# Kernel tuning notes

Hardware: AMD Instinct MI355X
Metric: run time of the kernel (lower is better)

## Reference

```python
import jax, jax.numpy as jnp
import numpy as np

VOCAB = 32000
HID = 512
T_IN = 128
T_OUT = 128
BATCH = 32


def gru_scan(xs, h0, W, U, bi, br):
    """Keras GRUCell (reset_after=True) over time.
    xs: [T, B, H] inputs; h0: [B, H]; W: [H, 3H]; U: [H, 3H]; bi, br: [3H].
    Returns (h_final [B,H], hs [T,B,H])."""
    # input projections for all timesteps at once
    x_proj = jnp.einsum('tbh,hg->tbg', xs, W) + bi  # [T, B, 3H]

    def step(h, xp):
        rec = h @ U + br                      # [B, 3H]
        xz, xr, xh = jnp.split(xp, 3, axis=-1)
        rz, rr, rh = jnp.split(rec, 3, axis=-1)
        z = jax.nn.sigmoid(xz + rz)
        r = jax.nn.sigmoid(xr + rr)
        hh = jnp.tanh(xh + r * rh)
        h_new = z * h + (1.0 - z) * hh
        return h_new, h_new

    h_final, hs = jax.lax.scan(step, h0, x_proj)
    return h_final, hs


def setup_inputs() -> dict:
    key = jax.random.key(0)
    ks = jax.random.split(key, 12)
    s = 0.05
    return {
        'inputs': jax.random.randint(ks[0], (BATCH, T_IN), 0, VOCAB, dtype=jnp.int64 if jax.config.jax_enable_x64 else jnp.int32),
        'emb': jax.random.normal(ks[1], (VOCAB, HID), jnp.float32) * s,
        'enc_W': jax.random.normal(ks[2], (HID, 3 * HID), jnp.float32) * s,
        'enc_U': jax.random.normal(ks[3], (HID, 3 * HID), jnp.float32) * s,
        'enc_bi': jnp.zeros((3 * HID,), jnp.float32),
        'enc_br': jnp.zeros((3 * HID,), jnp.float32),
        'dec_W': jax.random.normal(ks[4], (HID, 3 * HID), jnp.float32) * s,
        'dec_U': jax.random.normal(ks[5], (HID, 3 * HID), jnp.float32) * s,
        'dec_bi': jnp.zeros((3 * HID,), jnp.float32),
        'dec_br': jnp.zeros((3 * HID,), jnp.float32),
        'w_relu': jax.random.normal(ks[6], (HID, HID), jnp.float32) * s,
        'b_relu': jnp.zeros((HID,), jnp.float32),
        'w_out': jax.random.normal(ks[7], (HID, VOCAB), jnp.float32) * s,
        'b_out': jnp.zeros((VOCAB,), jnp.float32),
    }


def reference(inputs, emb, enc_W, enc_U, enc_bi, enc_br,
              dec_W, dec_U, dec_bi, dec_br, w_relu, b_relu, w_out, b_out):
    B = inputs.shape[0]
    # Embedding lookup: [B, T_in, H] -> time-major [T_in, B, H]
    x = jnp.transpose(emb[inputs], (1, 0, 2))
    h0 = jnp.zeros((B, HID), jnp.float32)
    # Encoder GRU -> final state
    h_enc, _ = gru_scan(x, h0, enc_W, enc_U, enc_bi, enc_br)
    # RepeatVector: decoder input is encoder state at every target step
    dec_in = jnp.broadcast_to(h_enc[None], (T_OUT, B, HID))
    # Decoder GRU with fresh zero state, return sequences
    _, hs = gru_scan(dec_in, h0, dec_W, dec_U, dec_bi, dec_br)  # [T_out, B, H]
    hs = jnp.transpose(hs, (1, 0, 2))  # [B, T_out, H]
    # TimeDistributed Dense+relu, then Dense+softmax over vocab
    h1 = jax.nn.relu(jnp.einsum('bth,hk->btk', hs, w_relu) + b_relu)
    logits = jnp.einsum('bth,hv->btv', h1, w_out) + b_out
    return jax.nn.softmax(logits, axis=-1)
```

## Files before the change

### kernel.cpp

```cpp
#include <hip/hip_runtime.h>
#include <stdint.h>

#define VOCAB 32000
#define HID   512
#define G3    1536
#define TT    128
#define BB    32
#define NROW  4096
#define NCB   250

typedef __attribute__((ext_vector_type(8))) short short8;
typedef __attribute__((ext_vector_type(4))) short short4v;
typedef __attribute__((ext_vector_type(4))) float f32x4;
typedef __attribute__((ext_vector_type(2))) unsigned long long u64x2;

__device__ __forceinline__ unsigned short f2bf(float f) {
  unsigned int u = __builtin_bit_cast(unsigned int, f);
  u += 0x7fffu + ((u >> 16) & 1u);
  return (unsigned short)(u >> 16);
}
__device__ __forceinline__ float bf2f(unsigned short s) {
  unsigned int u = ((unsigned int)s) << 16;
  return __builtin_bit_cast(float, u);
}
__device__ __forceinline__ void gload16(const void* g, void* l) {
  __builtin_amdgcn_global_load_lds(
      (const __attribute__((address_space(1))) unsigned int*)g,
      (__attribute__((address_space(3))) unsigned int*)l, 16, 0, 0);
}
__device__ __forceinline__ unsigned long long AL64(const unsigned long long* p) {
  return __hip_atomic_load(p, __ATOMIC_RELAXED, __HIP_MEMORY_SCOPE_AGENT);
}
__device__ __forceinline__ unsigned int AL32(const unsigned int* p) {
  return __hip_atomic_load(p, __ATOMIC_RELAXED, __HIP_MEMORY_SCOPE_AGENT);
}
__device__ __forceinline__ void AS64(unsigned long long* p, unsigned long long v) {
  __hip_atomic_store(p, v, __ATOMIC_RELAXED, __HIP_MEMORY_SCOPE_AGENT);
}
__device__ __forceinline__ void AS32(unsigned int* p, unsigned int v) {
  __hip_atomic_store(p, v, __ATOMIC_RELAXED, __HIP_MEMORY_SCOPE_AGENT);
}

__global__ void transpose_bf16_k(const float* __restrict__ src,
                                 unsigned short* __restrict__ dst,
                                 int K, int N) {
  __shared__ float t[64][65];
  int k0 = blockIdx.x * 64, n0 = blockIdx.y * 64;
  int c = threadIdx.x & 15, rr = threadIdx.x >> 4;
#pragma unroll
  for (int i = 0; i < 4; ++i) {
    float4 v = *(const float4*)(src + (size_t)(k0 + rr + 16 * i) * N + n0 + c * 4);
    t[rr + 16 * i][c * 4 + 0] = v.x;
    t[rr + 16 * i][c * 4 + 1] = v.y;
    t[rr + 16 * i][c * 4 + 2] = v.z;
    t[rr + 16 * i][c * 4 + 3] = v.w;
  }
  __syncthreads();
#pragma unroll
  for (int i = 0; i < 4; ++i) {
    short4v o;
#pragma unroll
    for (int j = 0; j < 4; ++j) o[j] = (short)f2bf(t[c * 4 + j][rr + 16 * i]);
    *(short4v*)(dst + (size_t)(n0 + rr + 16 * i) * K + k0 + c * 4) = o;
  }
}

__global__ void embed_k(const int* __restrict__ inputs,
                        const float* __restrict__ emb,
                        unsigned short* __restrict__ xb) {
  int r = blockIdx.x;
  int t = r >> 5, b = r & 31;
  int idx = inputs[b * TT + t];
  const float* src = emb + (size_t)idx * HID;
  unsigned short* dst = xb + (size_t)r * HID;
  int j = threadIdx.x * 4;
  float4 v = *(const float4*)(src + j);
  short4v o;
  o[0] = (short)f2bf(v.x); o[1] = (short)f2bf(v.y);
  o[2] = (short)f2bf(v.z); o[3] = (short)f2bf(v.w);
  *(short4v*)(dst + j) = o;
}

template<int MODE>
__launch_bounds__(256)
__global__ void gemm_bt(const unsigned short* __restrict__ A,
                        const unsigned short* __restrict__ BT,
                        const float* __restrict__ bias,
                        void* __restrict__ Cv,
                        float* __restrict__ partials,
                        int M, int N, int K) {
  __shared__ unsigned short As[8192];
  __shared__ unsigned short Bs[8192];
  __shared__ float rsum[2][128];
  int tid = threadIdx.x;
  int l = tid & 63;
  int w = tid >> 6;
  int wm = w >> 1, wn = w & 1;

  int nwg = (int)(gridDim.x * gridDim.y);
  int id = (int)(blockIdx.y * gridDim.x + blockIdx.x);
  int nid = (id & 7) * (nwg >> 3) + (id >> 3);
  int bx = nid & 31, by = nid >> 5;
  int row0 = bx * 128;
  int col0 = by * 128;

  int sr = (w << 5) + (l >> 3);
  int sg = ((l & 7) ^ ((l >> 3) & 7)) << 3;
  const unsigned short* Ag = A  + (size_t)(row0 + sr) * K + sg;
  const unsigned short* Bg = BT + (size_t)(col0 + sr) * K + sg;

  int cA = l & 15, q = l >> 4, x7 = l & 7;
  const char* asp = (const char*)As;
  const char* bsp = (const char*)Bs;

  f32x4 acc[4][4];
#pragma unroll
  for (int m = 0; m < 4; ++m)
#pragma unroll
    for (int n = 0; n < 4; ++n) acc[m][n] = (f32x4){0.f, 0.f, 0.f, 0.f};

  for (int k0 = 0; k0 < K; k0 += 64) {
    if (k0) __syncthreads();
#pragma unroll
    for (int i = 0; i < 4; ++i) {
      gload16(Ag + (size_t)(i * 8) * K + k0, As + ((w << 2) + i) * 512);
      gload16(Bg + (size_t)(i * 8) * K + k0, Bs + ((w << 2) + i) * 512);
    }
    __syncthreads();
#pragma unroll
    for (int kk = 0; kk < 2; ++kk) {
      int sl = (((kk << 2) + q) ^ x7) << 4;
      short8 af[4], bf[4];
#pragma unroll
      for (int m = 0; m < 4; ++m)
        af[m] = *(const short8*)(asp + (wm * 64 + m * 16 + cA) * 128 + sl);
#pragma unroll
      for (int n = 0; n < 4; ++n)
        bf[n] = *(const short8*)(bsp + (wn * 64 + n * 16 + cA) * 128 + sl);
#pragma unroll
      for (int m = 0; m < 4; ++m)
#pragma unroll
        for (int n = 0; n < 4; ++n)
          acc[m][n] = __builtin_amdgcn_mfma_f32_16x16x32_bf16(af[m], bf[n],
                                                              acc[m][n], 0, 0, 0);
    }
  }

  if (MODE == 0 || MODE == 1) {
#pragma unroll
    for (int m = 0; m < 4; ++m)
#pragma unroll
      for (int n = 0; n < 4; ++n) {
        int col = col0 + wn * 64 + n * 16 + cA;
        float bv = bias[col];
#pragma unroll
        for (int r = 0; r < 4; ++r) {
          int row = row0 + wm * 64 + m * 16 + q * 4 + r;
          float v = acc[m][n][r] + bv;
          if (MODE == 0)
            ((float*)Cv)[(size_t)row * N + col] = v;
          else
            ((unsigned short*)Cv)[(size_t)row * N + col] = f2bf(fmaxf(v, 0.f));
        }
      }
  } else {
    float ps[4][4];
#pragma unroll
    for (int m = 0; m < 4; ++m)
#pragma unroll
      for (int r = 0; r < 4; ++r) ps[m][r] = 0.f;
#pragma unroll
    for (int m = 0; m < 4; ++m)
#pragma unroll
      for (int n = 0; n < 4; ++n) {
        int col = col0 + wn * 64 + n * 16 + cA;
        float bv = bias[col];
#pragma unroll
        for (int r = 0; r < 4; ++r) {
          int row = row0 + wm * 64 + m * 16 + q * 4 + r;
          float lv = acc[m][n][r] + bv;
          float v = __expf(lv);
          if (MODE == 2)
            ((float*)Cv)[(size_t)row * N + col] = v;
          else
            ((unsigned short*)Cv)[(size_t)row * N + col] = f2bf(lv);
          ps[m][r] += v;
        }
      }
#pragma unroll
    for (int mask = 1; mask < 16; mask <<= 1)
#pragma unroll
      for (int m = 0; m < 4; ++m)
#pragma unroll
        for (int r = 0; r < 4; ++r)
          ps[m][r] += __shfl_xor(ps[m][r], mask, 64);
    if (cA == 0) {
#pragma unroll
      for (int m = 0; m < 4; ++m)
#pragma unroll
        for (int r = 0; r < 4; ++r)
          rsum[wn][wm * 64 + m * 16 + q * 4 + r] = ps[m][r];
    }
    __syncthreads();
    if (tid < 128)
      partials[(size_t)by * NROW + row0 + tid] = rsum[0][tid] + rsum[1][tid];
  }
}

__launch_bounds__(256)
__global__ void gemm_small_k(const unsigned short* __restrict__ A,
                             const unsigned short* __restrict__ B,
                             const float* __restrict__ bias,
                             float* __restrict__ C,
                             int M, int N, int K) {
  __shared__ unsigned short As[64][56];
  __shared__ unsigned short Bs[64][56];
  int tid = threadIdx.x;
  int lane = tid & 63;
  int w = tid >> 6;
  int wm = w >> 1, wn = w & 1;
  int row0 = blockIdx.x * 64;
  int n0 = blockIdx.y * 64;
  f32x4 acc[2][2];
#pragma unroll
  for (int a = 0; a < 2; ++a)
#pragma unroll
    for (int c = 0; c < 2; ++c) acc[a][c] = (f32x4){0.f, 0.f, 0.f, 0.f};
  for (int k0 = 0; k0 < K; k0 += 32) {
    {
      int row = tid >> 2;
      int kg = (tid & 3) * 8;
      short8 v = {};
      if (row0 + row < M)
        v = *(const short8*)(A + (size_t)(row0 + row) * K + k0 + kg);
      *(short8*)&As[row][kg] = v;
    }
    {
      int k = tid >> 3;
      int ng = (tid & 7) * 8;
      short8 v = *(const short8*)(B + (size_t)(k0 + k) * N + n0 + ng);
#pragma unroll
      for (int qq = 0; qq < 8; ++qq) Bs[ng + qq][k] = (unsigned short)v[qq];
    }
    __syncthreads();
    int kb = (lane >> 4) * 8;
    short8 af0 = *(const short8*)&As[wm * 32 + (lane & 15)][kb];
    short8 af1 = *(const short8*)&As[wm * 32 + 16 + (lane & 15)][kb];
    short8 bf0 = *(const short8*)&Bs[wn * 32 + (lane & 15)][kb];
    short8 bf1 = *(const short8*)&Bs[wn * 32 + 16 + (lane & 15)][kb];
    acc[0][0] = __builtin_amdgcn_mfma_f32_16x16x32_bf16(af0, bf0, acc[0][0], 0, 0, 0);
    acc[0][1] = __builtin_amdgcn_mfma_f32_16x16x32_bf16(af0, bf1, acc[0][1], 0, 0, 0);
    acc[1][0] = __builtin_amdgcn_mfma_f32_16x16x32_bf16(af1, bf0, acc[1][0], 0, 0, 0);
    acc[1][1] = __builtin_amdgcn_mfma_f32_16x16x32_bf16(af1, bf1, acc[1][1], 0, 0, 0);
    __syncthreads();
  }
#pragma unroll
  for (int tm = 0; tm < 2; ++tm)
#pragma unroll
    for (int tn = 0; tn < 2; ++tn) {
      int col = n0 + wn * 32 + tn * 16 + (lane & 15);
      float bv = bias[col];
#pragma unroll
      for (int r = 0; r < 4; ++r) {
        int row = row0 + wm * 32 + tm * 16 + ((lane >> 4) * 4) + r;
        if (row < M)
          C[(size_t)row * N + col] = acc[tm][tn][r] + bv;
      }
    }
}

template<int XPT>
__device__ void gru_body(char* smem, const float* __restrict__ U,
                         const float* __restrict__ xp, const float* __restrict__ br,
                         unsigned short* __restrict__ hpub,
                         unsigned int* __restrict__ flags) {
  unsigned short* ub = (unsigned short*)smem;
  char* hbase = smem + 49152;
  float (*recbuf)[32][16] = (float (*)[32][16])(smem + 81920);
  int tid = threadIdx.x;
  int lane = tid & 63;
  int w = tid >> 6;
  int g = blockIdx.x;

  for (int idx = tid; idx < 16 * 3 * 64 * 8; idx += 512) {
    int i = idx & 7;
    int l = (idx >> 3) & 63;
    int rem = idx >> 9;
    int nt = rem % 3;
    int ks = rem / 3;
    int k = ks * 32 + ((l >> 4) * 8) + i;
    int col = nt * 512 + g * 16 + (l & 15);
    ub[idx] = f2bf(U[(size_t)k * G3 + col]);
  }
  int b = tid >> 4, j = tid & 15;
  float br_z = br[g * 16 + j];
  float br_r = br[512 + g * 16 + j];
  float br_h = br[1024 + g * 16 + j];
  float hreg = 0.f;
  __syncthreads();

  int mt = w / 3, nt = w % 3;
  for (int t = 0; t < TT; ++t) {
    size_t xbase = ((size_t)(t * XPT + b)) * G3 + g * 16 + j;
    float xz = xp[xbase], xr = xp[xbase + 512], xh = xp[xbase + 1024];

    float rz, rr, rh;
    if (t == 0) {
      rz = 0.f; rr = 0.f; rh = 0.f;
    } else {
      {
        const unsigned long long* hr =
            (const unsigned long long*)(hpub + ((t & 1) ? 16384 : 0));
        int r = tid >> 4, s = tid & 15;
        unsigned long long av[8];
#pragma unroll
        for (int k = 0; k < 4; ++k) {
          const unsigned long long* p = hr + (size_t)r * 128 + (s + 16 * k) * 2;
          av[2 * k] = AL64(p);
          av[2 * k + 1] = AL64(p + 1);
        }
        int rx = (r & 7) << 4;
#pragma unroll
        for (int k = 0; k < 4; ++k) {
          int wb = (r * 1024 + (s + 16 * k) * 16) ^ rx;
          u64x2 v;
          v[0] = av[2 * k];
          v[1] = av[2 * k + 1];
          *(u64x2*)(hbase + wb) = v;
        }
      }
      __syncthreads();

      if (w < 6) {
        int arow = mt * 16 + (lane & 15);
        int rx = (arow & 7) << 4;
        int abase = arow * 1024 + (lane >> 4) * 16;
        f32x4 acc0 = (f32x4){0.f, 0.f, 0.f, 0.f};
        f32x4 acc1 = (f32x4){0.f, 0.f, 0.f, 0.f};
#pragma unroll
        for (int ks = 0; ks < 8; ++ks) {
          short8 af0 = *(const short8*)(hbase + ((abase + ks * 64) ^ rx));
          short8 af1 = *(const short8*)(hbase + ((abase + (ks + 8) * 64) ^ rx));
          short8 bf0 = *(const short8*)&ub[((ks * 3 + nt) * 64 + lane) * 8];
          short8 bf1 = *(const short8*)&ub[(((ks + 8) * 3 + nt) * 64 + lane) * 8];
          acc0 = __builtin_amdgcn_mfma_f32_16x16x32_bf16(af0, bf0, acc0, 0, 0, 0);
          acc1 = __builtin_amdgcn_mfma_f32_16x16x32_bf16(af1, bf1, acc1, 0, 0, 0);
        }
        f32x4 acc = acc0 + acc1;
#pragma unroll
        for (int r = 0; r < 4; ++r)
          recbuf[nt][mt * 16 + (lane >> 4) * 4 + r][lane & 15] = acc[r];
      }
      __syncthreads();
      rz = recbuf[0][b][j];
      rr = recbuf[1][b][j];
      rh = recbuf[2][b][j];
    }

    float z = 1.f / (1.f + __expf(-(xz + rz + br_z)));
    float rg = 1.f / (1.f + __expf(-(xr + rr + br_r)));
    float pre = xh + rg * (rh + br_h);
    pre = fminf(fmaxf(pre, -15.f), 15.f);
    float e2 = __expf(2.f * pre);
    float hh = (e2 - 1.f) / (e2 + 1.f);
    hreg = z * hreg + (1.f - z) * hh;
    unsigned short hb = f2bf(hreg);

    unsigned int hv = (unsigned int)hb;
    unsigned int p1 = (unsigned int)__shfl_xor((int)hv, 1, 64);
    unsigned long long lo = (unsigned long long)((hv & 0xffffu) | (p1 << 16));
    unsigned long long hi =
        (unsigned long long)(unsigned int)__shfl_xor((int)(unsigned int)lo, 2, 64);
    if ((j & 3) == 0) {
      unsigned long long pk = (lo & 0xffffffffull) | (hi << 32);
      AS64((unsigned long long*)(hpub + (((t + 1) & 1) ? 16384 : 0) +
                                 b * HID + g * 16 + j), pk);
    }

    if (t + 1 < TT) {
      asm volatile("s_waitcnt vmcnt(0)" ::: "memory");
      __syncthreads();
      if (tid == 0)
        AS32(flags + g * 32, (unsigned)(t + 1));
      if (lane < 32) {
        const unsigned int* fp = flags + lane * 32;
        while (AL32(fp) < (unsigned)(t + 1)) {}
      }
    }
  }
}

__launch_bounds__(512)
__global__ void gru_k(const float* __restrict__ U,
                      const float* __restrict__ xp,
                      const float* __restrict__ br,
                      unsigned short* __restrict__ hpub,
                      unsigned short* __restrict__ hsout,
                      unsigned int* __restrict__ flags) {
  __shared__ unsigned short ub[16 * 3 * 64 * 8];
  __shared__ unsigned short hbuf[16384];
  __shared__ float recbuf[3][32][16];
  int tid = threadIdx.x;
  int lane = tid & 63;
  int w = tid >> 6;
  int g = blockIdx.x;
  char* hbase = (char*)hbuf;

  for (int idx = tid; idx < 16 * 3 * 64 * 8; idx += 512) {
    int i = idx & 7;
    int l = (idx >> 3) & 63;
    int rem = idx >> 9;
    int nt = rem % 3;
    int ks = rem / 3;
    int k = ks * 32 + ((l >> 4) * 8) + i;
    int col = nt * 512 + g * 16 + (l & 15);
    ub[idx] = f2bf(U[(size_t)k * G3 + col]);
  }
  int b = tid >> 4, j = tid & 15;
  float br_z = br[g * 16 + j];
  float br_r = br[512 + g * 16 + j];
  float br_h = br[1024 + g * 16 + j];
  float hreg = 0.f;
  __syncthreads();

  int mt = w / 3, nt = w % 3;
  for (int t = 0; t < TT; ++t) {
    size_t xbase = ((size_t)b) * G3 + g * 16 + j;
    float xz = xp[xbase], xr = xp[xbase + 512], xh = xp[xbase + 1024];

    float rz, rr, rh;
    if (t == 0) {
      rz = 0.f; rr = 0.f; rh = 0.f;
    } else {
      {
        const unsigned long long* hr =
            (const unsigned long long*)(hpub + ((t & 1) ? 16384 : 0));
        int r = tid >> 4, s = tid & 15;
        unsigned long long av[8];
#pragma unroll
        for (int k = 0; k < 4; ++k) {
          const unsigned long long* p = hr + (size_t)r * 128 + (s + 16 * k) * 2;
          av[2 * k] = AL64(p);
          av[2 * k + 1] = AL64(p + 1);
        }
        int rx = (r & 7) << 4;
#pragma unroll
        for (int k = 0; k < 4; ++k) {
          int wb = (r * 1024 + (s + 16 * k) * 16) ^ rx;
          u64x2 v;
          v[0] = av[2 * k];
          v[1] = av[2 * k + 1];
          *(u64x2*)(hbase + wb) = v;
        }
      }
      __syncthreads();

      if (w < 6) {
        int arow = mt * 16 + (lane & 15);
        int rx = (arow & 7) << 4;
        int abase = arow * 1024 + (lane >> 4) * 16;
        f32x4 acc0 = (f32x4){0.f, 0.f, 0.f, 0.f};
        f32x4 acc1 = (f32x4){0.f, 0.f, 0.f, 0.f};
#pragma unroll
        for (int ks = 0; ks < 8; ++ks) {
          short8 af0 = *(const short8*)(hbase + ((abase + ks * 64) ^ rx));
          short8 af1 = *(const short8*)(hbase + ((abase + (ks + 8) * 64) ^ rx));
          short8 bf0 = *(const short8*)&ub[((ks * 3 + nt) * 64 + lane) * 8];
          short8 bf1 = *(const short8*)&ub[(((ks + 8) * 3 + nt) * 64 + lane) * 8];
          acc0 = __builtin_amdgcn_mfma_f32_16x16x32_bf16(af0, bf0, acc0, 0, 0, 0);
          acc1 = __builtin_amdgcn_mfma_f32_16x16x32_bf16(af1, bf1, acc1, 0, 0, 0);
        }
        f32x4 acc = acc0 + acc1;
#pragma unroll
        for (int r = 0; r < 4; ++r)
          recbuf[nt][mt * 16 + (lane >> 4) * 4 + r][lane & 15] = acc[r];
      }
      __syncthreads();
      rz = recbuf[0][b][j];
      rr = recbuf[1][b][j];
      rh = recbuf[2][b][j];
    }

    float z = 1.f / (1.f + __expf(-(xz + rz + br_z)));
    float rg = 1.f / (1.f + __expf(-(xr + rr + br_r)));
    float pre = xh + rg * (rh + br_h);
    pre = fminf(fmaxf(pre, -15.f), 15.f);
    float e2 = __expf(2.f * pre);
    float hh = (e2 - 1.f) / (e2 + 1.f);
    hreg = z * hreg + (1.f - z) * hh;
    unsigned short hb = f2bf(hreg);

    unsigned int hv = (unsigned int)hb;
    unsigned int p1 = (unsigned int)__shfl_xor((int)hv, 1, 64);
    unsigned long long lo = (unsigned long long)((hv & 0xffffu) | (p1 << 16));
    unsigned long long hi =
        (unsigned long long)(unsigned int)__shfl_xor((int)(unsigned int)lo, 2, 64);
    if ((j & 3) == 0) {
      unsigned long long pk = (lo & 0xffffffffull) | (hi << 32);
      AS64((unsigned long long*)(hpub + (((t + 1) & 1) ? 16384 : 0) +
                                 b * HID + g * 16 + j), pk);
    }

    if (t + 1 < TT) {
      asm volatile("s_waitcnt vmcnt(0)" ::: "memory");
      __syncthreads();
      if (tid == 0)
        AS32(flags + g * 32, (unsigned)(t + 1));
    }
    hsout[((size_t)b * TT + t) * HID + g * 16 + j] = hb;
    if (t + 1 < TT) {
      if (lane < 32) {
        const unsigned int* fp = flags + lane * 32;
        while (AL32(fp) < (unsigned)(t + 1)) {}
      }
    }
  }
}

__device__ void tr_tile(char* sm, int tid8, const float* __restrict__ src,
                        unsigned short* __restrict__ dst,
                        int K, int N, int k0, int n0) {
  float (*t)[65] = (float (*)[65])sm;
  int c = tid8 & 15, rr = tid8 >> 4;
#pragma unroll
  for (int i = 0; i < 4; ++i) {
    float4 v = *(const float4*)(src + (size_t)(k0 + rr + 16 * i) * N + n0 + c * 4);
    t[rr + 16 * i][c * 4 + 0] = v.x;
    t[rr + 16 * i][c * 4 + 1] = v.y;
    t[rr + 16 * i][c * 4 + 2] = v.z;
    t[rr + 16 * i][c * 4 + 3] = v.w;
  }
  __syncthreads();
#pragma unroll
  for (int i = 0; i < 4; ++i) {
    short4v o;
#pragma unroll
    for (int j = 0; j < 4; ++j) o[j] = (short)f2bf(t[c * 4 + j][rr + 16 * i]);
    *(short4v*)(dst + (size_t)(n0 + rr + 16 * i) * K + k0 + c * 4) = o;
  }
}

__launch_bounds__(512)
__global__ void enc_fused_k(const float* __restrict__ U,
                            const float* __restrict__ xp,
                            const float* __restrict__ br,
                            unsigned short* __restrict__ hpub,
                            unsigned int* __restrict__ flags,
                            const float* __restrict__ w_out,
                            unsigned short* __restrict__ woutbT,
                            const float* __restrict__ w_relu,
                            unsigned short* __restrict__ wrelubT,
                            const float* __restrict__ decW,
                            unsigned short* __restrict__ decWb) {
  __shared__ char smem[88064];
  if (blockIdx.x < 32) {
    gru_body<32>(smem, U, xp, br, hpub, flags);
    return;
  }
  int tid = threadIdx.x;
  int wid = (int)blockIdx.x - 32;
  int eng = tid >> 8, tid8 = tid & 255;
  char* sm = smem + eng * 36864;
  for (int it = 0; it < 10; ++it) {
    int tk = wid * 2 + eng + it * 448;
    if (tk < 4000) {
      tr_tile(sm, tid8, w_out, woutbT, 512, VOCAB, (tk & 7) * 64, (tk >> 3) * 64);
    } else if (tk < 4064) {
      int t2 = tk - 4000;
      tr_tile(sm, tid8, w_relu, wrelubT, 512, 512, (t2 & 7) * 64, (t2 >> 3) * 64);
    } else if (tk < 4448) {
      int c = tk - 4064;
      int base = c * 2048 + tid8 * 8;
      float4 a = *(const float4*)(decW + base);
      float4 bq = *(const float4*)(decW + base + 4);
      short8 o;
      o[0] = (short)f2bf(a.x); o[1] = (short)f2bf(a.y);
      o[2] = (short)f2bf(a.z); o[3] = (short)f2bf(a.w);
      o[4] = (short)f2bf(bq.x); o[5] = (short)f2bf(bq.y);
      o[6] = (short)f2bf(bq.z); o[7] = (short)f2bf(bq.w);
      *(short8*)(decWb + base) = o;
      __syncthreads();
    } else {
      __syncthreads();
    }
  }
}

__global__ void rowsum_k(const float* __restrict__ part, float* __restrict__ inv) {
  int r = blockIdx.x * blockDim.x + threadIdx.x;
  float s = 0.f;
  for (int c = 0; c < NCB; ++c) s += part[(size_t)c * NROW + r];
  inv[r] = 1.f / s;
}

__global__ void norm2_k(const unsigned short* __restrict__ lg,
                        const float* __restrict__ inv,
                        float* __restrict__ out) {
  const unsigned int C8 = VOCAB / 8;
  const unsigned int total8 = (unsigned int)NROW * C8;
  unsigned int stride = gridDim.x * blockDim.x;
  for (unsigned int i = blockIdx.x * blockDim.x + threadIdx.x; i < total8;
       i += stride) {
    unsigned int r = i / C8;
    float s = inv[r];
    short8 v = *(const short8*)(lg + (size_t)i * 8);
    float4 a, b;
    a.x = __expf(bf2f((unsigned short)v[0])) * s;
    a.y = __expf(bf2f((unsigned short)v[1])) * s;
    a.z = __expf(bf2f((unsigned short)v[2])) * s;
    a.w = __expf(bf2f((unsigned short)v[3])) * s;
    b.x = __expf(bf2f((unsigned short)v[4])) * s;
    b.y = __expf(bf2f((unsigned short)v[5])) * s;
    b.z = __expf(bf2f((unsigned short)v[6])) * s;
    b.w = __expf(bf2f((unsigned short)v[7])) * s;
    *(float4*)(out + (size_t)i * 8) = a;
    *(float4*)(out + (size_t)i * 8 + 4) = b;
  }
}

extern "C" void kernel_launch(void* const* d_in, const int* in_sizes, int n_in,
                              void* d_out, int out_size, void* d_ws, size_t ws_size,
                              hipStream_t stream) {
  const int*   inputs = (const int*)d_in[0];
  const float* emb    = (const float*)d_in[1];
  const float* encW   = (const float*)d_in[2];
  const float* encU   = (const float*)d_in[3];
  const float* enc_bi = (const float*)d_in[4];
  const float* enc_br = (const float*)d_in[5];
  const float* decW   = (const float*)d_in[6];
  const float* decU   = (const float*)d_in[7];
  const float* dec_bi = (const float*)d_in[8];
  const float* dec_br = (const float*)d_in[9];
  const float* w_relu = (const float*)d_in[10];
  const float* b_relu = (const float*)d_in[11];
  const float* w_out  = (const float*)d_in[12];
  const float* b_out  = (const float*)d_in[13];

  char* ws = (char*)d_ws;
  const size_t o_xproj  = 0;
  const size_t o_xb     = 25165824;
  const size_t o_encWbT = 29360128;
  const size_t o_decWb  = 30932992;
  const size_t o_wrelubT= 32505856;
  const size_t o_woutbT = 33030144;
  const size_t o_decxp  = 65798144;
  const size_t o_hsb    = 65994752;
  const size_t o_h1b    = 70189056;
  const size_t o_part   = 74383360;
  const size_t o_inv    = 82575360;
  const size_t o_hpubE  = 82591744;
  const size_t o_hpubD  = 82657280;
  const size_t o_logit  = 82722816;

  float*          xproj   = (float*)(ws + o_xproj);
  unsigned short* xb      = (unsigned short*)(ws + o_xb);
  unsigned short* encWbT  = (unsigned short*)(ws + o_encWbT);
  unsigned short* decWb   = (unsigned short*)(ws + o_decWb);
  unsigned short* wrelubT = (unsigned short*)(ws + o_wrelubT);
  unsigned short* woutbT  = (unsigned short*)(ws + o_woutbT);
  float*          decxp   = (float*)(ws + o_decxp);
  unsigned short* hsb     = (unsigned short*)(ws + o_hsb);
  unsigned short* h1b     = (unsigned short*)(ws + o_h1b);
  float*          part    = (float*)(ws + o_part);
  float*          inv     = (float*)(ws + o_inv);
  unsigned short* hpubE   = (unsigned short*)(ws + o_hpubE);
  unsigned short* hpubD   = (unsigned short*)(ws + o_hpubD);
  unsigned short* logit   = (unsigned short*)(ws + o_logit);
  unsigned int*   flagsE  = (unsigned int*)(ws + o_part);
  unsigned int*   flagsD  = (unsigned int*)(ws + o_part + 4096);

  (void)hipMemsetAsync(ws + o_part, 0, 8192, stream);
  (void)hipMemsetAsync(ws + o_hpubE, 0, 131072, stream);

  transpose_bf16_k<<<dim3(8, 24), 256, 0, stream>>>(encW, encWbT, HID, G3);
  embed_k<<<4096, 128, 0, stream>>>(inputs, emb, xb);

  gemm_bt<0><<<dim3(32, 12), 256, 0, stream>>>(xb, encWbT, enc_bi, xproj,
                                               nullptr, NROW, G3, HID);

  enc_fused_k<<<256, 512, 0, stream>>>(encU, xproj, enc_br, hpubE, flagsE,
                                       w_out, woutbT, w_relu, wrelubT,
                                       decW, decWb);

  gemm_small_k<<<dim3(1, 24), 256, 0, stream>>>(hpubE, decWb, dec_bi, decxp,
                                                BB, G3, HID);

  gru_k<<<32, 512, 0, stream>>>(decU, decxp, dec_br, hpubD, hsb, flagsD);

  gemm_bt<1><<<dim3(32, 4), 256, 0, stream>>>(hsb, wrelubT, b_relu, h1b,
                                              nullptr, NROW, HID, HID);
  gemm_bt<3><<<dim3(32, NCB), 256, 0, stream>>>(h1b, woutbT, b_out, logit,
                                                part, NROW, VOCAB, HID);
  rowsum_k<<<16, 256, 0, stream>>>(part, inv);
  norm2_k<<<2048, 256, 0, stream>>>(logit, inv, (float*)d_out);
}
```

Measured before the change: 1.261 ms.

## Fuse embedding gather into encoder input projection GEMM, add s_sleep to spin waits

Replaces the separate embedding kernel and bf16 staging buffer with a GEMM that gathers embedding rows directly, converts them to bf16 on the fly and writes them into shared memory. This removes one launch and a global round trip for the activation matrix. It also adds s_sleep in the inter-block flag spin loops to cut memory polling pressure, and drops the hpubE memset. Risks are that synchronous A loads are no longer asynchronous like the B loads, and that sleeping adds wake-up latency on the recurrent critical path.

```diff
diff --git a/kernel.cpp b/kernel.cpp
--- a/kernel.cpp
+++ b/kernel.cpp
@@ -65,20 +65,100 @@
   }
 }
 
-__global__ void embed_k(const int* __restrict__ inputs,
-                        const float* __restrict__ emb,
-                        unsigned short* __restrict__ xb) {
-  int r = blockIdx.x;
-  int t = r >> 5, b = r & 31;
-  int idx = inputs[b * TT + t];
-  const float* src = emb + (size_t)idx * HID;
-  unsigned short* dst = xb + (size_t)r * HID;
-  int j = threadIdx.x * 4;
-  float4 v = *(const float4*)(src + j);
-  short4v o;
-  o[0] = (short)f2bf(v.x); o[1] = (short)f2bf(v.y);
-  o[2] = (short)f2bf(v.z); o[3] = (short)f2bf(v.w);
-  *(short4v*)(dst + j) = o;
+__launch_bounds__(256)
+__global__ void gemm_embed_proj(const int* __restrict__ inputs,
+                                const float* __restrict__ emb,
+                                const unsigned short* __restrict__ BT,
+                                const float* __restrict__ bias,
+                                float* __restrict__ C,
+                                int M, int N, int K) {
+  __shared__ unsigned short As[8192];
+  __shared__ unsigned short Bs[8192];
+  int tid = threadIdx.x;
+  int l = tid & 63;
+  int w = tid >> 6;
+  int wm = w >> 1, wn = w & 1;
+  int nwg = (int)(gridDim.x * gridDim.y);
+  int id = (int)(blockIdx.y * gridDim.x + blockIdx.x);
+  int nid = (id & 7) * (nwg >> 3) + (id >> 3);
+  int bx = nid & 31, by = nid >> 5;
+  int row0 = bx * 128, col0 = by * 128;
+
+  int sr = (w << 5) + (l >> 3);
+  int sg = ((l & 7) ^ ((l >> 3) & 7)) << 3;
+  const float* Ag0;
+  const float* Ag1;
+  const float* Ag2;
+  const float* Ag3;
+  {
+    int R0 = row0 + sr;
+    const float* a[4];
+#pragma unroll
+    for (int i = 0; i < 4; ++i) {
+      int R = R0 + i * 8;
+      int tt = R >> 5, b = R & 31;
+      int idx = inputs[b * TT + tt];
+      a[i] = emb + (size_t)idx * HID + sg;
+    }
+    Ag0 = a[0]; Ag1 = a[1]; Ag2 = a[2]; Ag3 = a[3];
+  }
+  const unsigned short* Bg = BT + (size_t)(col0 + sr) * K + sg;
+  int cA = l & 15, q = l >> 4, x7 = l & 7;
+  const char* asp = (const char*)As;
+  const char* bsp = (const char*)Bs;
+
+  f32x4 acc[4][4];
+#pragma unroll
+  for (int m = 0; m < 4; ++m)
+#pragma unroll
+    for (int n = 0; n < 4; ++n) acc[m][n] = (f32x4){0.f, 0.f, 0.f, 0.f};
+
+  for (int k0 = 0; k0 < K; k0 += 64) {
+    if (k0) __syncthreads();
+    const float* ap[4] = {Ag0 + k0, Ag1 + k0, Ag2 + k0, Ag3 + k0};
+#pragma unroll
+    for (int i = 0; i < 4; ++i) {
+      float4 a = *(const float4*)(ap[i]);
+      float4 b4 = *(const float4*)(ap[i] + 4);
+      short8 o;
+      o[0] = (short)f2bf(a.x);  o[1] = (short)f2bf(a.y);
+      o[2] = (short)f2bf(a.z);  o[3] = (short)f2bf(a.w);
+      o[4] = (short)f2bf(b4.x); o[5] = (short)f2bf(b4.y);
+      o[6] = (short)f2bf(b4.z); o[7] = (short)f2bf(b4.w);
+      *(short8*)((char*)As + (w * 4 + i) * 1024 + l * 16) = o;
+      gload16(Bg + (size_t)(i * 8) * K + k0, Bs + ((w << 2) + i) * 512);
+    }
+    __syncthreads();
+#pragma unroll
+    for (int kk = 0; kk < 2; ++kk) {
+      int sl = (((kk << 2) + q) ^ x7) << 4;
+      short8 af[4], bf[4];
+#pragma unroll
+      for (int m = 0; m < 4; ++m)
+        af[m] = *(const short8*)(asp + (wm * 64 + m * 16 + cA) * 128 + sl);
+#pragma unroll
+      for (int n = 0; n < 4; ++n)
+        bf[n] = *(const short8*)(bsp + (wn * 64 + n * 16 + cA) * 128 + sl);
+#pragma unroll
+      for (int m = 0; m < 4; ++m)
+#pragma unroll
+        for (int n = 0; n < 4; ++n)
+          acc[m][n] = __builtin_amdgcn_mfma_f32_16x16x32_bf16(af[m], bf[n],
+                                                              acc[m][n], 0, 0, 0);
+    }
+  }
+#pragma unroll
+  for (int m = 0; m < 4; ++m)
+#pragma unroll
+    for (int n = 0; n < 4; ++n) {
+      int col = col0 + wn * 64 + n * 16 + cA;
+      float bv = bias[col];
+#pragma unroll
+      for (int r = 0; r < 4; ++r) {
+        int row = row0 + wm * 64 + m * 16 + q * 4 + r;
+        C[(size_t)row * N + col] = acc[m][n][r] + bv;
+      }
+    }
 }
 
 template<int MODE>
@@ -146,7 +226,7 @@
     }
   }
 
-  if (MODE == 0 || MODE == 1) {
+  if (MODE == 1) {
 #pragma unroll
     for (int m = 0; m < 4; ++m)
 #pragma unroll
@@ -157,10 +237,7 @@
         for (int r = 0; r < 4; ++r) {
           int row = row0 + wm * 64 + m * 16 + q * 4 + r;
           float v = acc[m][n][r] + bv;
-          if (MODE == 0)
-            ((float*)Cv)[(size_t)row * N + col] = v;
-          else
-            ((unsigned short*)Cv)[(size_t)row * N + col] = f2bf(fmaxf(v, 0.f));
+          ((unsigned short*)Cv)[(size_t)row * N + col] = f2bf(fmaxf(v, 0.f));
         }
       }
   } else {
@@ -180,10 +257,7 @@
           int row = row0 + wm * 64 + m * 16 + q * 4 + r;
           float lv = acc[m][n][r] + bv;
           float v = __expf(lv);
-          if (MODE == 2)
-            ((float*)Cv)[(size_t)row * N + col] = v;
-          else
-            ((unsigned short*)Cv)[(size_t)row * N + col] = f2bf(lv);
+          ((unsigned short*)Cv)[(size_t)row * N + col] = f2bf(lv);
           ps[m][r] += v;
         }
       }
@@ -384,7 +458,7 @@
         AS32(flags + g * 32, (unsigned)(t + 1));
       if (lane < 32) {
         const unsigned int* fp = flags + lane * 32;
-        while (AL32(fp) < (unsigned)(t + 1)) {}
+        while (AL32(fp) < (unsigned)(t + 1)) __builtin_amdgcn_s_sleep(1);
       }
     }
   }
@@ -511,7 +585,7 @@
     if (t + 1 < TT) {
       if (lane < 32) {
         const unsigned int* fp = flags + lane * 32;
-        while (AL32(fp) < (unsigned)(t + 1)) {}
+        while (AL32(fp) < (unsigned)(t + 1)) __builtin_amdgcn_s_sleep(1);
       }
     }
   }
@@ -653,7 +727,6 @@
   const size_t o_logit  = 82722816;
 
   float*          xproj   = (float*)(ws + o_xproj);
-  unsigned short* xb      = (unsigned short*)(ws + o_xb);
   unsigned short* encWbT  = (unsigned short*)(ws + o_encWbT);
   unsigned short* decWb   = (unsigned short*)(ws + o_decWb);
   unsigned short* wrelubT = (unsigned short*)(ws + o_wrelubT);
@@ -668,15 +741,15 @@
   unsigned short* logit   = (unsigned short*)(ws + o_logit);
   unsigned int*   flagsE  = (unsigned int*)(ws + o_part);
   unsigned int*   flagsD  = (unsigned int*)(ws + o_part + 4096);
+  (void)o_xb;
 
   (void)hipMemsetAsync(ws + o_part, 0, 8192, stream);
-  (void)hipMemsetAsync(ws + o_hpubE, 0, 131072, stream);
 
   transpose_bf16_k<<<dim3(8, 24), 256, 0, stream>>>(encW, encWbT, HID, G3);
-  embed_k<<<4096, 128, 0, stream>>>(inputs, emb, xb);
-
-  gemm_bt<0><<<dim3(32, 12), 256, 0, stream>>>(xb, encWbT, enc_bi, xproj,
-                                               nullptr, NROW, G3, HID);
+
+  gemm_embed_proj<<<dim3(32, 12), 256, 0, stream>>>(inputs, emb, encWbT,
+                                                    enc_bi, xproj,
+                                                    NROW, G3, HID);
 
   enc_fused_k<<<256, 512, 0, stream>>>(encU, xproj, enc_br, hpubE, flagsE,
                                        w_out, woutbT, w_relu, wrelubT,
```

After: 1.291 ms. 2.4% more time.
